# Optimization experiments

Hardware: AMD Instinct MI355X
Metric: run time of the kernel (lower is better)

## Reference

```python
import jax, jax.numpy as jnp
import numpy as np

B, S, H, D = 4, 1024, 20, 64
DM = H * D          # 1280 model dim
DF = 4 * DM         # 5120 ffn dim
EPS = 1e-5          # haiku LayerNorm default


def setup_inputs() -> dict:
    key = jax.random.key(0)
    ks = jax.random.split(key, 12)
    sc = 1.0 / np.sqrt(DM)
    return {
        "x": jax.random.normal(ks[0], (B, S, DM), jnp.float32),
        "ln1_scale": jnp.ones((DM,), jnp.float32),
        "ln1_offset": jnp.zeros((DM,), jnp.float32),
        "wq": jax.random.normal(ks[1], (DM, DM), jnp.float32) * sc,
        "bq": jnp.zeros((DM,), jnp.float32),
        "wk": jax.random.normal(ks[2], (DM, DM), jnp.float32) * sc,
        "bk": jnp.zeros((DM,), jnp.float32),
        "wv": jax.random.normal(ks[3], (DM, DM), jnp.float32) * sc,
        "bv": jnp.zeros((DM,), jnp.float32),
        "wo": jax.random.normal(ks[4], (DM, DM), jnp.float32) * sc,
        "bo": jnp.zeros((DM,), jnp.float32),
        "ln2_scale": jnp.ones((DM,), jnp.float32),
        "ln2_offset": jnp.zeros((DM,), jnp.float32),
        "fc1_w": jax.random.normal(ks[5], (DM, DF), jnp.float32) * sc,
        "fc1_b": jnp.zeros((DF,), jnp.float32),
        "fc2_w": jax.random.normal(ks[6], (DF, DM), jnp.float32) * (1.0 / np.sqrt(DF)),
        "fc2_b": jnp.zeros((DM,), jnp.float32),
    }


def _layer_norm(x, scale, offset):
    m = jnp.mean(x, axis=-1, keepdims=True)
    v = jnp.mean(jnp.square(x - m), axis=-1, keepdims=True)
    return (x - m) * jax.lax.rsqrt(v + EPS) * scale + offset


def reference(x, ln1_scale, ln1_offset, wq, bq, wk, bk, wv, bv, wo, bo,
              ln2_scale, ln2_offset, fc1_w, fc1_b, fc2_w, fc2_b):
    b, s, dm = x.shape
    # --- self-attention sub-block ---
    res = x
    h = _layer_norm(x, ln1_scale, ln1_offset)
    q = (h @ wq + bq).reshape(b, s, H, D)
    k = (h @ wk + bk).reshape(b, s, H, D)
    v = (h @ wv + bv).reshape(b, s, H, D)
    logits = jnp.einsum('bthd,bThd->bhtT', q, k) / jnp.sqrt(jnp.asarray(D, x.dtype))
    weights = jax.nn.softmax(logits, axis=-1)
    attn = jnp.einsum('bhtT,bThd->bthd', weights, v).reshape(b, s, dm)
    x = res + (attn @ wo + bo)
    # --- MLP sub-block ---
    res = x
    h = _layer_norm(x, ln2_scale, ln2_offset)
    h = jax.nn.gelu(h @ fc1_w + fc1_b, approximate=False)
    x = res + (h @ fc2_w + fc2_b)
    return x
```

## Files before the change

### kernel.cpp

```cpp
#include <hip/hip_runtime.h>
#include <hip/hip_bf16.h>

typedef __hip_bfloat16 bf16;
typedef __attribute__((ext_vector_type(8))) short short8;
typedef __attribute__((ext_vector_type(4))) float f32x4;
typedef __attribute__((ext_vector_type(4))) unsigned short u16x4;

#define DMODEL 1280
#define DFFN   5120
#define BATCH  4
#define SEQ    1024
#define NHEAD  20
#define HDIM   64
#define NROWS  (BATCH * SEQ)

#define GLDS(g, l) __builtin_amdgcn_global_load_lds(                            \
    (const __attribute__((address_space(1))) void*)(g),                         \
    (__attribute__((address_space(3))) void*)(l), 16, 0, 0)

__global__ __launch_bounds__(256) void prep_all(
    const float* __restrict__ wq, const float* __restrict__ wk,
    const float* __restrict__ wv, const float* __restrict__ wo,
    const float* __restrict__ fc1w, const float* __restrict__ fc2w,
    const float* __restrict__ bq, const float* __restrict__ bk,
    const float* __restrict__ bv,
    bf16* __restrict__ wqkvt, bf16* __restrict__ wot,
    bf16* __restrict__ fc1t, bf16* __restrict__ fc2t,
    float* __restrict__ bqkv)
{
    const int bid = blockIdx.x;
    if (bid == 19200) {
        for (int i = threadIdx.x; i < DMODEL; i += 256) {
            bqkv[i]              = bq[i];
            bqkv[DMODEL + i]     = bk[i];
            bqkv[2 * DMODEL + i] = bv[i];
        }
        return;
    }
    const float* in;
    bf16* out;
    int K, N, n0, k0;
    if (bid < 6400) {
        const int mat = bid / 1600, rem = bid % 1600;
        K = DMODEL; N = DMODEL;
        n0 = (rem % 40) * 32; k0 = (rem / 40) * 32;
        switch (mat) {
            case 0:  in = wq; out = wqkvt; break;
            case 1:  in = wk; out = wqkvt + (size_t)DMODEL * DMODEL; break;
            case 2:  in = wv; out = wqkvt + (size_t)2 * DMODEL * DMODEL; break;
            default: in = wo; out = wot; break;
        }
    } else if (bid < 12800) {
        const int rem = bid - 6400;
        K = DMODEL; N = DFFN; in = fc1w; out = fc1t;
        n0 = (rem % 160) * 32; k0 = (rem / 160) * 32;
    } else {
        const int rem = bid - 12800;
        K = DFFN; N = DMODEL; in = fc2w; out = fc2t;
        n0 = (rem % 40) * 32; k0 = (rem / 40) * 32;
    }
    __shared__ float tile[32][33];
    const int tx = threadIdx.x & 31;
    const int ty = threadIdx.x >> 5;
    for (int i = 0; i < 32; i += 8)
        tile[ty + i][tx] = in[(size_t)(k0 + ty + i) * N + (n0 + tx)];
    __syncthreads();
    for (int i = 0; i < 32; i += 8)
        out[(size_t)(n0 + ty + i) * K + (k0 + tx)] = __float2bfloat16(tile[tx][ty + i]);
}

__global__ __launch_bounds__(256) void ln_bf16(
    const float* __restrict__ x, const float* __restrict__ sc,
    const float* __restrict__ of, bf16* __restrict__ out)
{
    const int row = blockIdx.x;
    const float* xr = x + (size_t)row * DMODEL;
    float v[5];
    float s = 0.f, s2 = 0.f;
    for (int i = 0; i < 5; ++i) {
        v[i] = xr[threadIdx.x + i * 256];
        s += v[i];
        s2 += v[i] * v[i];
    }
    for (int off = 1; off < 64; off <<= 1) {
        s  += __shfl_xor(s, off);
        s2 += __shfl_xor(s2, off);
    }
    __shared__ float red[2][4];
    const int wid = threadIdx.x >> 6;
    if ((threadIdx.x & 63) == 0) { red[0][wid] = s; red[1][wid] = s2; }
    __syncthreads();
    s  = red[0][0] + red[0][1] + red[0][2] + red[0][3];
    s2 = red[1][0] + red[1][1] + red[1][2] + red[1][3];
    const float mean = s * (1.0f / DMODEL);
    const float var  = s2 * (1.0f / DMODEL) - mean * mean;
    const float rstd = rsqrtf(var + 1e-5f);
    for (int i = 0; i < 5; ++i) {
        const int c = threadIdx.x + i * 256;
        const float y = (v[i] - mean) * rstd * sc[c] + of[c];
        out[(size_t)row * DMODEL + c] = __float2bfloat16(y);
    }
}

__global__ __launch_bounds__(256) void reduce2_ln(
    const float* __restrict__ P, const float* __restrict__ bias,
    const float* __restrict__ res, float* __restrict__ x1,
    const float* __restrict__ sc, const float* __restrict__ of,
    bf16* __restrict__ h2)
{
    const int row = blockIdx.x;
    const size_t base = (size_t)row * DMODEL;
    const int MN = NROWS * DMODEL;
    float v[5];
    float s = 0.f, s2 = 0.f;
    for (int i = 0; i < 5; ++i) {
        const int c = threadIdx.x + i * 256;
        const float val = P[base + c] + P[MN + base + c] + bias[c] + res[base + c];
        v[i] = val;
        x1[base + c] = val;
        s += val;
        s2 += val * val;
    }
    for (int off = 1; off < 64; off <<= 1) {
        s  += __shfl_xor(s, off);
        s2 += __shfl_xor(s2, off);
    }
    __shared__ float red[2][4];
    const int wid = threadIdx.x >> 6;
    if ((threadIdx.x & 63) == 0) { red[0][wid] = s; red[1][wid] = s2; }
    __syncthreads();
    s  = red[0][0] + red[0][1] + red[0][2] + red[0][3];
    s2 = red[1][0] + red[1][1] + red[1][2] + red[1][3];
    const float mean = s * (1.0f / DMODEL);
    const float var  = s2 * (1.0f / DMODEL) - mean * mean;
    const float rstd = rsqrtf(var + 1e-5f);
    for (int i = 0; i < 5; ++i) {
        const int c = threadIdx.x + i * 256;
        const float y = (v[i] - mean) * rstd * sc[c] + of[c];
        h2[base + c] = __float2bfloat16(y);
    }
}

template <int EPI>
__global__ __launch_bounds__(256, 4) void gemm_bf16(
    const bf16* __restrict__ A, const bf16* __restrict__ Bt,
    const float* __restrict__ bias,
    bf16* __restrict__ Cb, float* __restrict__ Cf,
    int M, int N, int K, int klen)
{
    __shared__ bf16 As[2][128][32];
    __shared__ bf16 Bs[2][128][32];
    const int m0 = blockIdx.x * 128;
    const int n0 = blockIdx.y * 128;
    const int z  = blockIdx.z;
    const int kbeg = z * klen;

    const int tid  = threadIdx.x;
    const int lane = tid & 63;
    const int wid  = tid >> 6;
    const int wm   = (wid >> 1) * 64;
    const int wn   = (wid & 1) * 64;
    const int l15  = lane & 15;
    const int lq   = lane >> 4;

    f32x4 acc[4][4];
    for (int i = 0; i < 4; ++i)
        for (int j = 0; j < 4; ++j)
            acc[i][j] = (f32x4){0.f, 0.f, 0.f, 0.f};

    const int srow = lane >> 2;
    const int cph  = lane & 3;
    const int cgl8 = (cph ^ ((srow >> 1) & 3)) * 8;
    const int lrow = wid * 16 + srow;
    const int lcol = cph * 8;

    const bf16* aT = A  + (size_t)(m0 + lrow) * K + kbeg + cgl8;
    const bf16* bT = Bt + (size_t)(n0 + lrow) * K + kbeg + cgl8;
    const size_t rstep = (size_t)64 * K;

    GLDS(aT,         &As[0][lrow][lcol]);
    GLDS(aT + rstep, &As[0][lrow + 64][lcol]);
    GLDS(bT,         &Bs[0][lrow][lcol]);
    GLDS(bT + rstep, &Bs[0][lrow + 64][lcol]);

    const int ca = (lq ^ ((l15 >> 1) & 3)) * 8;
    const int nIter = klen / 32;
    for (int it = 0; it < nIter; ++it) {
        const int buf = it & 1;
        __syncthreads();
        if (it + 1 < nIter) {
            const int k1 = (it + 1) * 32;
            GLDS(aT + k1,         &As[buf ^ 1][lrow][lcol]);
            GLDS(aT + k1 + rstep, &As[buf ^ 1][lrow + 64][lcol]);
            GLDS(bT + k1,         &Bs[buf ^ 1][lrow][lcol]);
            GLDS(bT + k1 + rstep, &Bs[buf ^ 1][lrow + 64][lcol]);
        }
        short8 af[4], bfr[4];
        for (int mt = 0; mt < 4; ++mt)
            af[mt] = *(const short8*)(&As[buf][wm + mt * 16 + l15][ca]);
        for (int nt = 0; nt < 4; ++nt)
            bfr[nt] = *(const short8*)(&Bs[buf][wn + nt * 16 + l15][ca]);
        for (int mt = 0; mt < 4; ++mt)
            for (int nt = 0; nt < 4; ++nt)
                acc[mt][nt] = __builtin_amdgcn_mfma_f32_16x16x32_bf16(
                    af[mt], bfr[nt], acc[mt][nt], 0, 0, 0);
    }

    float* Pf = Cf + (size_t)z * M * N;
    for (int mt = 0; mt < 4; ++mt)
        for (int nt = 0; nt < 4; ++nt)
            for (int r = 0; r < 4; ++r) {
                const int row = m0 + wm + mt * 16 + lq * 4 + r;
                const int col = n0 + wn + nt * 16 + l15;
                if (EPI == 0) {
                    const float v = acc[mt][nt][r] + bias[col];
                    Cb[(size_t)row * N + col] = __float2bfloat16(v);
                } else if (EPI == 2) {
                    const float v = acc[mt][nt][r] + bias[col];
                    const float g = 0.5f * v * (1.0f + erff(v * 0.70710678118654752f));
                    Cb[(size_t)row * N + col] = __float2bfloat16(g);
                } else {
                    Pf[(size_t)row * N + col] = acc[mt][nt][r];
                }
            }
}

__global__ __launch_bounds__(256) void reduce2(
    const float* __restrict__ P, const float* __restrict__ bias,
    const float* __restrict__ res, float* __restrict__ out, int MN, int N)
{
    const int i = (blockIdx.x * 256 + threadIdx.x) * 4;
    if (i >= MN) return;
    const float4 p0 = *(const float4*)(P + i);
    const float4 p1 = *(const float4*)(P + MN + i);
    const float4 r  = *(const float4*)(res + i);
    const float4 b  = *(const float4*)(bias + (i % N));
    float4 o;
    o.x = p0.x + p1.x + r.x + b.x;
    o.y = p0.y + p1.y + r.y + b.y;
    o.z = p0.z + p1.z + r.z + b.z;
    o.w = p0.w + p1.w + r.w + b.w;
    *(float4*)(out + i) = o;
}

__global__ __launch_bounds__(256) void flash_attn(
    const bf16* __restrict__ qb, const bf16* __restrict__ kb,
    const bf16* __restrict__ vb, bf16* __restrict__ ob, int ldq)
{
    __shared__ bf16 Ks[2][64][64];
    __shared__ bf16 Vt[64][64];
    __shared__ bf16 Ps[4][16][64];

    const int bh = blockIdx.y;
    const int b  = bh / NHEAD;
    const int hh = bh % NHEAD;
    const int q0 = blockIdx.x * 64;
    const int tid  = threadIdx.x;
    const int lane = tid & 63;
    const int wid  = tid >> 6;
    const int l15  = lane & 15;
    const int lq   = lane >> 4;
    const int key  = l15 & 7;

    short8 qf[2];
    {
        const bf16* qp = qb + (size_t)(b * SEQ + q0 + wid * 16 + l15) * ldq
                         + hh * HDIM + lq * 8;
        for (int kk = 0; kk < 2; ++kk) {
            union { short8 v; bf16 h[8]; } u;
            u.v = *(const short8*)(qp + kk * 32);
            for (int j = 0; j < 8; ++j)
                u.h[j] = __float2bfloat16(__bfloat162float(u.h[j]) * 0.125f);
            qf[kk] = u.v;
        }
    }

    f32x4 o[4];
    for (int dt = 0; dt < 4; ++dt) o[dt] = (f32x4){0.f, 0.f, 0.f, 0.f};
    float lsum = 0.f;

    const int krow  = wid * 8 + (lane >> 3);
    const int kcgl8 = ((lane & 7) ^ (krow & 7)) * 8;
    const int kcph8 = (lane & 7) * 8;
    const int vd0  = (tid & 15) * 4;
    const int vkv0 = (tid >> 4) * 4;

    const bf16* kBase = kb + (size_t)(b * SEQ + krow) * ldq + hh * HDIM + kcgl8;
    const bf16* vBase = vb + (size_t)(b * SEQ + vkv0) * ldq + hh * HDIM + vd0;

    GLDS(kBase,                    &Ks[0][krow][kcph8]);
    GLDS(kBase + (size_t)32 * ldq, &Ks[0][krow + 32][kcph8]);
    u16x4 vr[4];
    for (int j = 0; j < 4; ++j)
        vr[j] = *(const u16x4*)(vBase + (size_t)j * ldq);

    const int nIter = SEQ / 64;
    for (int it = 0; it < nIter; ++it) {
        const int buf = it & 1;
        __syncthreads();
        for (int i = 0; i < 4; ++i) {
            u16x4 w = { vr[0][i], vr[1][i], vr[2][i], vr[3][i] };
            const int p = ((vkv0 >> 3) ^ ((vd0 + i) & 7)) * 8 + (vkv0 & 7);
            *(u16x4*)(&Vt[vd0 + i][p]) = w;
        }
        __syncthreads();

        if (it + 1 < nIter) {
            const size_t off = (size_t)(it + 1) * 64 * ldq;
            GLDS(kBase + off,                    &Ks[buf ^ 1][krow][kcph8]);
            GLDS(kBase + off + (size_t)32 * ldq, &Ks[buf ^ 1][krow + 32][kcph8]);
            for (int j = 0; j < 4; ++j)
                vr[j] = *(const u16x4*)(vBase + off + (size_t)j * ldq);
        }

        for (int mt = 0; mt < 4; ++mt) {
            const bf16* kp = &Ks[buf][mt * 16 + l15][0];
            const short8 kf0 = *(const short8*)(kp + ((0 + lq) ^ key) * 8);
            const short8 kf1 = *(const short8*)(kp + ((4 + lq) ^ key) * 8);
            f32x4 a = (f32x4){0.f, 0.f, 0.f, 0.f};
            a = __builtin_amdgcn_mfma_f32_16x16x32_bf16(kf0, qf[0], a, 0, 0, 0);
            a = __builtin_amdgcn_mfma_f32_16x16x32_bf16(kf1, qf[1], a, 0, 0, 0);
            union { u16x4 v; bf16 h[4]; } pk;
            for (int r = 0; r < 4; ++r) {
                const float p = __expf(a[r]);
                lsum += p;
                pk.h[r] = __float2bfloat16(p);
            }
            const int pc = ((mt * 2 + (lq >> 1)) ^ key) * 8 + (lq & 1) * 4;
            *(u16x4*)(&Ps[wid][l15][pc]) = pk.v;
        }

        for (int kk = 0; kk < 2; ++kk) {
            const short8 pf = *(const short8*)(
                &Ps[wid][l15][((lq + 4 * kk) ^ key) * 8]);
            for (int dt = 0; dt < 4; ++dt) {
                const short8 vf = *(const short8*)(
                    &Vt[dt * 16 + l15][((lq + 4 * kk) ^ key) * 8]);
                o[dt] = __builtin_amdgcn_mfma_f32_16x16x32_bf16(
                    vf, pf, o[dt], 0, 0, 0);
            }
        }
    }

    lsum += __shfl_xor(lsum, 16);
    lsum += __shfl_xor(lsum, 32);
    const float inv_l = 1.0f / lsum;

    const size_t qrow = (size_t)(b * SEQ + q0 + wid * 16 + l15);
    for (int dt = 0; dt < 4; ++dt) {
        union { u16x4 v; bf16 h[4]; } w;
        for (int r = 0; r < 4; ++r)
            w.h[r] = __float2bfloat16(o[dt][r] * inv_l);
        *(u16x4*)(ob + qrow * DMODEL + hh * HDIM + dt * 16 + lq * 4) = w.v;
    }
}

extern "C" void kernel_launch(void* const* d_in, const int* in_sizes, int n_in,
                              void* d_out, int out_size, void* d_ws, size_t ws_size,
                              hipStream_t stream)
{
    (void)in_sizes; (void)n_in; (void)out_size; (void)ws_size;
    const float* x    = (const float*)d_in[0];
    const float* ln1s = (const float*)d_in[1];
    const float* ln1o = (const float*)d_in[2];
    const float* wq   = (const float*)d_in[3];
    const float* bq   = (const float*)d_in[4];
    const float* wk   = (const float*)d_in[5];
    const float* bk   = (const float*)d_in[6];
    const float* wv   = (const float*)d_in[7];
    const float* bv   = (const float*)d_in[8];
    const float* wo   = (const float*)d_in[9];
    const float* bo   = (const float*)d_in[10];
    const float* ln2s = (const float*)d_in[11];
    const float* ln2o = (const float*)d_in[12];
    const float* fc1w = (const float*)d_in[13];
    const float* fc1b = (const float*)d_in[14];
    const float* fc2w = (const float*)d_in[15];
    const float* fc2b = (const float*)d_in[16];
    float* out = (float*)d_out;

    char* wp = (char*)d_ws;
    auto alloc = [&](size_t n) { char* p = wp; wp += (n + 255) & ~(size_t)255; return p; };
    bf16*  wqkvt = (bf16*)alloc((size_t)3 * DMODEL * DMODEL * 2);
    bf16*  wot   = (bf16*)alloc((size_t)DMODEL * DMODEL * 2);
    bf16*  fc1t  = (bf16*)alloc((size_t)DFFN * DMODEL * 2);
    bf16*  fc2t  = (bf16*)alloc((size_t)DMODEL * DFFN * 2);
    float* bqkv  = (float*)alloc((size_t)3 * DMODEL * 4);
    char*  regA  = alloc((size_t)NROWS * DMODEL * 2
                       + (size_t)NROWS * 3 * DMODEL * 2
                       + (size_t)NROWS * DMODEL * 2);
    bf16*  h     = (bf16*)regA;
    bf16*  qkv   = (bf16*)(regA + (size_t)NROWS * DMODEL * 2);
    bf16*  attn  = (bf16*)(regA + (size_t)NROWS * 4 * DMODEL * 2);
    float* part  = (float*)regA;
    bf16*  h2    = (bf16*)alloc((size_t)NROWS * DMODEL * 2);
    bf16*  g     = (bf16*)alloc((size_t)NROWS * DFFN * 2);
    float* x1    = out;

    prep_all<<<19201, 256, 0, stream>>>(
        wq, wk, wv, wo, fc1w, fc2w, bq, bk, bv,
        wqkvt, wot, fc1t, fc2t, bqkv);

    ln_bf16<<<NROWS, 256, 0, stream>>>(x, ln1s, ln1o, h);

    gemm_bf16<0><<<dim3(NROWS / 128, 3 * DMODEL / 128, 1), 256, 0, stream>>>(
        h, wqkvt, bqkv, qkv, nullptr, NROWS, 3 * DMODEL, DMODEL, DMODEL);

    flash_attn<<<dim3(SEQ / 64, BATCH * NHEAD), 256, 0, stream>>>(
        qkv, qkv + DMODEL, qkv + 2 * DMODEL, attn, 3 * DMODEL);

    gemm_bf16<3><<<dim3(NROWS / 128, DMODEL / 128, 2), 256, 0, stream>>>(
        attn, wot, nullptr, nullptr, part, NROWS, DMODEL, DMODEL, DMODEL / 2);
    reduce2_ln<<<NROWS, 256, 0, stream>>>(part, bo, x, x1, ln2s, ln2o, h2);

    gemm_bf16<2><<<dim3(NROWS / 128, DFFN / 128, 1), 256, 0, stream>>>(
        h2, fc1t, fc1b, g, nullptr, NROWS, DFFN, DMODEL, DMODEL);

    gemm_bf16<3><<<dim3(NROWS / 128, DMODEL / 128, 2), 256, 0, stream>>>(
        g, fc2t, nullptr, nullptr, part, NROWS, DMODEL, DFFN, DFFN / 2);
    reduce2<<<(NROWS * DMODEL / 4 + 255) / 256, 256, 0, stream>>>(
        part, fc2b, x1, out, NROWS * DMODEL, DMODEL);
}
```

Before: 474.0 us.

## Add 256x256-tile triple-buffered GEMM for QKV, FC1 and FC2

Adds a new 512-thread GEMM kernel with 256x256 output tiles, a three-stage LDS pipeline built on global_load_lds, and s_setprio around the MFMA bursts. The QKV, FC1 and FC2 projections now use it in place of the 128x128 kernel. The larger tile raises arithmetic intensity and operand reuse, and the deeper prefetch hides more global-load latency. In exchange it uses more registers and LDS per block, and the grids get smaller (e.g. 16x5 blocks for FC2 with split 2, 16x15 for QKV), which can leave CUs idle.

```diff
diff --git a/kernel.cpp b/kernel.cpp
--- a/kernel.cpp
+++ b/kernel.cpp
@@ -209,6 +209,125 @@
     float* Pf = Cf + (size_t)z * M * N;
     for (int mt = 0; mt < 4; ++mt)
         for (int nt = 0; nt < 4; ++nt)
+            for (int r = 0; r < 4; ++r) {
+                const int row = m0 + wm + mt * 16 + lq * 4 + r;
+                const int col = n0 + wn + nt * 16 + l15;
+                if (EPI == 0) {
+                    const float v = acc[mt][nt][r] + bias[col];
+                    Cb[(size_t)row * N + col] = __float2bfloat16(v);
+                } else if (EPI == 2) {
+                    const float v = acc[mt][nt][r] + bias[col];
+                    const float g = 0.5f * v * (1.0f + erff(v * 0.70710678118654752f));
+                    Cb[(size_t)row * N + col] = __float2bfloat16(g);
+                } else {
+                    Pf[(size_t)row * N + col] = acc[mt][nt][r];
+                }
+            }
+}
+
+template <int EPI>
+__global__ __launch_bounds__(512, 2) void gemm256(
+    const bf16* __restrict__ A, const bf16* __restrict__ Bt,
+    const float* __restrict__ bias,
+    bf16* __restrict__ Cb, float* __restrict__ Cf,
+    int M, int N, int K, int klen)
+{
+    __shared__ bf16 As[3][256][32];
+    __shared__ bf16 Bs[3][256][32];
+    const int m0 = blockIdx.x * 256;
+    const int n0 = blockIdx.y * 256;
+    const int z  = blockIdx.z;
+    const int kbeg = z * klen;
+
+    const int tid  = threadIdx.x;
+    const int lane = tid & 63;
+    const int wid  = tid >> 6;
+    const int wm   = (wid >> 2) * 128;
+    const int wn   = (wid & 3) * 64;
+    const int l15  = lane & 15;
+    const int lq   = lane >> 4;
+
+    f32x4 acc[8][4];
+    #pragma unroll
+    for (int i = 0; i < 8; ++i)
+        #pragma unroll
+        for (int j = 0; j < 4; ++j)
+            acc[i][j] = (f32x4){0.f, 0.f, 0.f, 0.f};
+
+    const int cph  = lane & 3;
+    const int lrow = wid * 16 + (lane >> 2);
+    const int cgl8 = (cph ^ ((lrow >> 1) & 3)) * 8;
+    const int lcol = cph * 8;
+
+    const bf16* aT = A  + (size_t)(m0 + lrow) * K + kbeg + cgl8;
+    const bf16* bT = Bt + (size_t)(n0 + lrow) * K + kbeg + cgl8;
+    const size_t rstep = (size_t)128 * K;
+
+    GLDS(aT,              &As[0][lrow][lcol]);
+    GLDS(aT + rstep,      &As[0][lrow + 128][lcol]);
+    GLDS(bT,              &Bs[0][lrow][lcol]);
+    GLDS(bT + rstep,      &Bs[0][lrow + 128][lcol]);
+    GLDS(aT + 32,         &As[1][lrow][lcol]);
+    GLDS(aT + 32 + rstep, &As[1][lrow + 128][lcol]);
+    GLDS(bT + 32,         &Bs[1][lrow][lcol]);
+    GLDS(bT + 32 + rstep, &Bs[1][lrow + 128][lcol]);
+
+    const int ca = (lq ^ ((l15 >> 1) & 3)) * 8;
+    const int nIter = klen / 32;
+    int buf = 0;
+    for (int it = 0; it < nIter; ++it) {
+        if (it + 1 < nIter) asm volatile("s_waitcnt vmcnt(4)" ::: "memory");
+        else                asm volatile("s_waitcnt vmcnt(0)" ::: "memory");
+        __builtin_amdgcn_s_barrier();
+
+        if (it + 2 < nIter) {
+            int bnx = buf + 2; if (bnx >= 3) bnx -= 3;
+            const int k2 = (it + 2) * 32;
+            GLDS(aT + k2,         &As[bnx][lrow][lcol]);
+            GLDS(aT + k2 + rstep, &As[bnx][lrow + 128][lcol]);
+            GLDS(bT + k2,         &Bs[bnx][lrow][lcol]);
+            GLDS(bT + k2 + rstep, &Bs[bnx][lrow + 128][lcol]);
+        }
+
+        short8 bfr[4];
+        #pragma unroll
+        for (int nt = 0; nt < 4; ++nt)
+            bfr[nt] = *(const short8*)(&Bs[buf][wn + nt * 16 + l15][ca]);
+        short8 af[4];
+        #pragma unroll
+        for (int mt = 0; mt < 4; ++mt)
+            af[mt] = *(const short8*)(&As[buf][wm + mt * 16 + l15][ca]);
+        __builtin_amdgcn_s_setprio(1);
+        #pragma unroll
+        for (int mt = 0; mt < 4; ++mt)
+            #pragma unroll
+            for (int nt = 0; nt < 4; ++nt)
+                acc[mt][nt] = __builtin_amdgcn_mfma_f32_16x16x32_bf16(
+                    af[mt], bfr[nt], acc[mt][nt], 0, 0, 0);
+        __builtin_amdgcn_s_setprio(0);
+        __builtin_amdgcn_s_barrier();
+
+        #pragma unroll
+        for (int mt = 0; mt < 4; ++mt)
+            af[mt] = *(const short8*)(&As[buf][wm + (mt + 4) * 16 + l15][ca]);
+        __builtin_amdgcn_s_setprio(1);
+        #pragma unroll
+        for (int mt = 0; mt < 4; ++mt)
+            #pragma unroll
+            for (int nt = 0; nt < 4; ++nt)
+                acc[mt + 4][nt] = __builtin_amdgcn_mfma_f32_16x16x32_bf16(
+                    af[mt], bfr[nt], acc[mt + 4][nt], 0, 0, 0);
+        __builtin_amdgcn_s_setprio(0);
+
+        buf = (buf == 2) ? 0 : buf + 1;
+    }
+
+    float* Pf = Cf + (size_t)z * M * N;
+    #pragma unroll
+    for (int mt = 0; mt < 8; ++mt)
+        #pragma unroll
+        for (int nt = 0; nt < 4; ++nt)
+            #pragma unroll
             for (int r = 0; r < 4; ++r) {
                 const int row = m0 + wm + mt * 16 + lq * 4 + r;
                 const int col = n0 + wn + nt * 16 + l15;
@@ -403,7 +522,7 @@
 
     ln_bf16<<<NROWS, 256, 0, stream>>>(x, ln1s, ln1o, h);
 
-    gemm_bf16<0><<<dim3(NROWS / 128, 3 * DMODEL / 128, 1), 256, 0, stream>>>(
+    gemm256<0><<<dim3(NROWS / 256, 3 * DMODEL / 256, 1), 512, 0, stream>>>(
         h, wqkvt, bqkv, qkv, nullptr, NROWS, 3 * DMODEL, DMODEL, DMODEL);
 
     flash_attn<<<dim3(SEQ / 64, BATCH * NHEAD), 256, 0, stream>>>(
@@ -413,10 +532,10 @@
         attn, wot, nullptr, nullptr, part, NROWS, DMODEL, DMODEL, DMODEL / 2);
     reduce2_ln<<<NROWS, 256, 0, stream>>>(part, bo, x, x1, ln2s, ln2o, h2);
 
-    gemm_bf16<2><<<dim3(NROWS / 128, DFFN / 128, 1), 256, 0, stream>>>(
+    gemm256<2><<<dim3(NROWS / 256, DFFN / 256, 1), 512, 0, stream>>>(
         h2, fc1t, fc1b, g, nullptr, NROWS, DFFN, DMODEL, DMODEL);
 
-    gemm_bf16<3><<<dim3(NROWS / 128, DMODEL / 128, 2), 256, 0, stream>>>(
+    gemm256<3><<<dim3(NROWS / 256, DMODEL / 256, 2), 512, 0, stream>>>(
         g, fc2t, nullptr, nullptr, part, NROWS, DMODEL, DFFN, DFFN / 2);
     reduce2<<<(NROWS * DMODEL / 4 + 255) / 256, 256, 0, stream>>>(
         part, fc2b, x1, out, NROWS * DMODEL, DMODEL);
```

Result: slower. 568.7 us (+20.0%).
